# Optimization experiments

Measured on AMD Instinct MI355X. Metric: run time of the kernel, lower is better.

## Reference

```python
import jax, jax.numpy as jnp
import numpy as np

DIM = 768
HEADS = 12
HID = 3072  # mlp_ratio * dim
BATCH = 8
FRAMES = 16
GRID = 14
NTOK = GRID * GRID
LN_EPS = 1e-5
EPS = 1e-6


def setup_inputs() -> dict:
    key = jax.random.key(0)
    ks = jax.random.split(key, 8)
    w = lambda k, shape: jax.random.normal(k, shape, jnp.float32) * 0.02
    return {
        "x": jax.random.normal(ks[0], (BATCH * FRAMES, NTOK, DIM), jnp.float32),
        "ln1_w": jnp.ones((DIM,), jnp.float32),
        "ln1_b": jnp.zeros((DIM,), jnp.float32),
        "qkv_w": w(ks[1], (3 * DIM, DIM)),
        "proj_w": w(ks[2], (DIM, DIM)),
        "proj_b": jnp.zeros((DIM,), jnp.float32),
        "ln2_w": jnp.ones((DIM,), jnp.float32),
        "ln2_b": jnp.zeros((DIM,), jnp.float32),
        "fc1_w": w(ks[3], (HID, DIM)),
        "fc1_b": jnp.zeros((HID,), jnp.float32),
        "dw_w": w(ks[4], (HID, 1, 3, 3)),
        "dw_b": jnp.zeros((HID,), jnp.float32),
        "fc2_w": w(ks[5], (DIM, HID)),
        "fc2_b": jnp.zeros((DIM,), jnp.float32),
        "H": GRID,
        "W": GRID,
        "num_frames": FRAMES,
    }


def _layernorm(x, w, b):
    mu = jnp.mean(x, axis=-1, keepdims=True)
    var = jnp.mean(jnp.square(x - mu), axis=-1, keepdims=True)
    return (x - mu) * jax.lax.rsqrt(var + LN_EPS) * w + b


def _joint_ts_attention(xn, qkv_w, proj_w, proj_b, num_frames):
    # xn: (b*f, n, c)
    Bt, n, C = xn.shape
    h = HEADS
    e = C // h
    scale = e ** (-0.5)
    qkv = jnp.einsum('bnc,dc->bnd', xn, qkv_w).reshape(Bt, n, 3, h, e)
    q, k, v = qkv[:, :, 0], qkv[:, :, 1], qkv[:, :, 2]
    # ReLU feature map + scale offset
    q_ = jax.nn.relu(q) + scale
    k_ = jax.nn.relu(k) + scale
    b = Bt // num_frames
    m = num_frames * n  # joint time-space sequence length
    q_ = q_.reshape(b, m, h, e)
    k_ = k_.reshape(b, m, h, e)
    v_ = v.reshape(b, m, h, e)
    # kv_: (b, h, e, e)
    kv = jnp.einsum('bnhe,bnhd->bhed', k_, v_)
    k_sum = jnp.sum(k_, axis=1)  # (b, h, e)
    z = 1.0 / (jnp.einsum('bnhe,bhe->bnh', q_, k_sum) + EPS)  # (b, m, h)
    out = jnp.einsum('bnhe,bhed->bnhd', q_, kv) * z[..., None]  # (b, m, h, e)
    out = out.reshape(Bt, n, C)
    return jnp.einsum('bnc,dc->bnd', out, proj_w) + proj_b


def _dwconv(x, w, b, H, W):
    # x: (B, N, C) -> NCHW depthwise 3x3, pad 1
    Bn, n, c = x.shape
    xi = jnp.transpose(x, (0, 2, 1)).reshape(Bn, c, H, W)
    y = jax.lax.conv_general_dilated(
        xi, w, window_strides=(1, 1), padding=((1, 1), (1, 1)),
        dimension_numbers=('NCHW', 'OIHW', 'NCHW'), feature_group_count=c)
    y = y + b[None, :, None, None]
    return jnp.transpose(y.reshape(Bn, c, n), (0, 2, 1))


def reference(x, ln1_w, ln1_b, qkv_w, proj_w, proj_b, ln2_w, ln2_b,
              fc1_w, fc1_b, dw_w, dw_b, fc2_w, fc2_b, H, W, num_frames):
    # x = x + attn(norm1(x), num_frames)
    x = x + _joint_ts_attention(_layernorm(x, ln1_w, ln1_b), qkv_w, proj_w, proj_b, num_frames)
    # x = x + mlp(norm2(x), H, W)
    xn = _layernorm(x, ln2_w, ln2_b)
    hdn = jnp.einsum('bnc,hc->bnh', xn, fc1_w) + fc1_b
    hdn = _dwconv(hdn, dw_w, dw_b, H, W)
    hdn = jax.nn.gelu(hdn, approximate=False)
    out = jnp.einsum('bnh,ch->bnc', hdn, fc2_w) + fc2_b
    return x + out
```

## Files before the change

kernel.cpp:

```cpp
#include <hip/hip_runtime.h>

typedef unsigned short u16;
typedef unsigned int u32;

typedef __bf16 bf16x8 __attribute__((ext_vector_type(8)));
typedef float f32x4 __attribute__((ext_vector_type(4)));

#define DIM 768
#define HID 3072
#define NTOK 196
#define BT 128
#define NTOKENS (BT * NTOK)
#define MJ 3136
#define HEADS 12

#define SZ_WB   ((size_t)(2304*768 + 768*768 + 3072*768 + 768*3072) * 2)
#define SZ_XN   ((size_t)NTOKENS * DIM * 2)
#define SZ_QKV  ((size_t)NTOKENS * 2304 * 2)
#define SZ_X2   ((size_t)NTOKENS * DIM * 4)
#define SZ_HDN  ((size_t)NTOKENS * HID * 2)
#define SZ_KV   ((size_t)96 * 4096 * 4)
#define SZ_KS   ((size_t)96 * 64 * 4)
#define WS_NEED (SZ_WB + SZ_XN + SZ_QKV + SZ_X2 + SZ_HDN + SZ_KV + SZ_KS)

static void* g_buf = nullptr;

__device__ __forceinline__ float b2f(u16 u) {
  union { u32 i; float f; } x; x.i = ((u32)u) << 16; return x.f;
}
__device__ __forceinline__ u16 f2b(float f) {
  u32 x = __float_as_uint(f);
  return (u16)((x + 0x7fffu + ((x >> 16) & 1u)) >> 16);
}

__device__ __forceinline__ void gload_lds16(const u16* g, u16* l) {
  __builtin_amdgcn_global_load_lds(
      (const __attribute__((address_space(1))) u32*)g,
      (__attribute__((address_space(3))) u32*)l, 16, 0, 0);
}

__global__ __launch_bounds__(256) void cvt_f32_bf16(const float* __restrict__ in,
    u16* __restrict__ out, int n4)
{
  int i = blockIdx.x * 256 + threadIdx.x;
  if (i < n4) {
    float4 f = ((const float4*)in)[i];
    ushort4 r;
    r.x = f2b(f.x); r.y = f2b(f.y); r.z = f2b(f.z); r.w = f2b(f.w);
    ((ushort4*)out)[i] = r;
  }
}

__global__ __launch_bounds__(256) void zero_f32(float* __restrict__ p, int n) {
  int i = blockIdx.x * 256 + threadIdx.x;
  if (i < n) p[i] = 0.0f;
}

__global__ __launch_bounds__(256) void ln_kernel(const float* __restrict__ xin,
    const float* __restrict__ w, const float* __restrict__ b, u16* __restrict__ out)
{
  const int token = blockIdx.x * 4 + (threadIdx.x >> 6);
  const int lane = threadIdx.x & 63;
  float v[12];
  const float* x = xin + (size_t)token * DIM;
#pragma unroll
  for (int c = 0; c < 3; ++c) {
    float4 f = *(const float4*)(x + c * 256 + lane * 4);
    v[c*4+0] = f.x; v[c*4+1] = f.y; v[c*4+2] = f.z; v[c*4+3] = f.w;
  }
  float s = 0.f, sq = 0.f;
#pragma unroll
  for (int i = 0; i < 12; ++i) { s += v[i]; sq += v[i] * v[i]; }
#pragma unroll
  for (int off = 32; off > 0; off >>= 1) {
    s += __shfl_xor(s, off, 64);
    sq += __shfl_xor(sq, off, 64);
  }
  const float mean = s * (1.0f / 768.0f);
  const float var = sq * (1.0f / 768.0f) - mean * mean;
  const float rstd = rsqrtf(var + 1e-5f);
  u16* o = out + (size_t)token * DIM;
#pragma unroll
  for (int c = 0; c < 3; ++c) {
    float4 wv = *(const float4*)(w + c * 256 + lane * 4);
    float4 bv = *(const float4*)(b + c * 256 + lane * 4);
    ushort4 r;
    r.x = f2b((v[c*4+0] - mean) * rstd * wv.x + bv.x);
    r.y = f2b((v[c*4+1] - mean) * rstd * wv.y + bv.y);
    r.z = f2b((v[c*4+2] - mean) * rstd * wv.z + bv.z);
    r.w = f2b((v[c*4+3] - mean) * rstd * wv.w + bv.w);
    *(ushort4*)(o + c * 256 + lane * 4) = r;
  }
}

template<int MODE, int NXT, int NN, int KK>
__global__ __launch_bounds__(512, 2) void gemm8(
    const u16* __restrict__ A, const u16* __restrict__ W,
    const float* __restrict__ bias, const float* __restrict__ res,
    void* __restrict__ out)
{
  extern __shared__ char smem[];
  u16* As = (u16*)smem;
  u16* Bs = (u16*)(smem + 65536);

  const int t = threadIdx.x;
  const int l = t & 63;
  const int w = t >> 6;
  const int wm = w >> 2;
  const int wn = w & 3;

  constexpr int TOTAL = 98 * NXT;
  constexpr int Q8 = TOTAL >> 3;
  constexpr int R8 = TOTAL & 7;
  const int orig = blockIdx.x;
  const int xcd = orig & 7;
  const int idx = orig >> 3;
  const int wg = (xcd < R8) ? (xcd * (Q8 + 1) + idx)
                            : (R8 * (Q8 + 1) + (xcd - R8) * Q8 + idx);
  const int m0 = (wg / NXT) * 256;
  const int n0 = (wg % NXT) * 256;

  const int srow = w * 16 + (l >> 3);
  const int scol = ((l & 7) ^ (l >> 3)) * 8;
  const u16* gA = A + (size_t)(m0 + srow) * KK + scol;
  const u16* gB = W + (size_t)(n0 + srow) * KK + scol;
  u16* lA = As + w * 1024;
  u16* lB = Bs + w * 1024;

#define STAGE_A(bb, h, kt) do { \
    const u16* g_ = gA + (size_t)(h) * 128 * KK + (size_t)(kt) * 64; \
    u16* l_ = lA + (bb) * 16384 + (h) * 8192; \
    gload_lds16(g_, l_); \
    gload_lds16(g_ + (size_t)8 * KK, l_ + 512); } while (0)
#define STAGE_B(bb, h, kt) do { \
    const u16* g_ = gB + (size_t)(h) * 128 * KK + (size_t)(kt) * 64; \
    u16* l_ = lB + (bb) * 16384 + (h) * 8192; \
    gload_lds16(g_, l_); \
    gload_lds16(g_ + (size_t)8 * KK, l_ + 512); } while (0)

  const int lm = l & 15;
  const int qq = l >> 4;
  const int acol = (qq << 4) ^ ((l & 7) << 4);
  const int abase = (wm * 128 + lm) * 128 + acol;
  const int bbase = (wn * 64 + lm) * 128 + acol;

  f32x4 acc[8][4];
#pragma unroll
  for (int mi = 0; mi < 8; ++mi)
#pragma unroll
    for (int ni = 0; ni < 4; ++ni) acc[mi][ni] = (f32x4){0.f, 0.f, 0.f, 0.f};

  constexpr int NT = KK / 64;

  STAGE_A(0, 0, 0); STAGE_A(0, 1, 0); STAGE_B(0, 0, 0); STAGE_B(0, 1, 0);
  STAGE_A(1, 0, 1); STAGE_A(1, 1, 1);
  asm volatile("s_waitcnt vmcnt(4)" ::: "memory");
  __builtin_amdgcn_s_barrier();

  for (int ti = 0; ti < NT; ++ti) {
    const int cb = ti & 1, nb = cb ^ 1;
    const char* Ac = (const char*)As + cb * 32768;
    const char* Bc = (const char*)Bs + cb * 32768;
    bf16x8 am[4][2], b01[2][2], b23[2][2];

#pragma unroll
    for (int mi = 0; mi < 4; ++mi) {
      const int off = abase + mi * 2048;
      am[mi][0] = *(const bf16x8*)(Ac + off);
      am[mi][1] = *(const bf16x8*)(Ac + (off ^ 64));
    }
#pragma unroll
    for (int ni = 0; ni < 2; ++ni) {
      const int off = bbase + ni * 2048;
      b01[ni][0] = *(const bf16x8*)(Bc + off);
      b01[ni][1] = *(const bf16x8*)(Bc + (off ^ 64));
    }
    if (ti + 1 < NT) STAGE_B(nb, 0, ti + 1);
    asm volatile("" ::: "memory");
    __builtin_amdgcn_s_barrier();
    asm volatile("s_waitcnt lgkmcnt(0)" ::: "memory");
    __builtin_amdgcn_s_setprio(1);
#pragma unroll
    for (int mi = 0; mi < 4; ++mi)
#pragma unroll
      for (int ni = 0; ni < 2; ++ni) {
        acc[mi][ni] = __builtin_amdgcn_mfma_f32_16x16x32_bf16(am[mi][0], b01[ni][0], acc[mi][ni], 0, 0, 0);
        acc[mi][ni] = __builtin_amdgcn_mfma_f32_16x16x32_bf16(am[mi][1], b01[ni][1], acc[mi][ni], 0, 0, 0);
      }
    __builtin_amdgcn_s_setprio(0);
    asm volatile("" ::: "memory");
    __builtin_amdgcn_s_barrier();

#pragma unroll
    for (int ni = 0; ni < 2; ++ni) {
      const int off = bbase + (ni + 2) * 2048;
      b23[ni][0] = *(const bf16x8*)(Bc + off);
      b23[ni][1] = *(const bf16x8*)(Bc + (off ^ 64));
    }
    if (ti + 1 < NT) STAGE_B(nb, 1, ti + 1);
    asm volatile("" ::: "memory");
    __builtin_amdgcn_s_barrier();
    asm volatile("s_waitcnt lgkmcnt(0)" ::: "memory");
    __builtin_amdgcn_s_setprio(1);
#pragma unroll
    for (int mi = 0; mi < 4; ++mi)
#pragma unroll
      for (int ni = 0; ni < 2; ++ni) {
        acc[mi][ni + 2] = __builtin_amdgcn_mfma_f32_16x16x32_bf16(am[mi][0], b23[ni][0], acc[mi][ni + 2], 0, 0, 0);
        acc[mi][ni + 2] = __builtin_amdgcn_mfma_f32_16x16x32_bf16(am[mi][1], b23[ni][1], acc[mi][ni + 2], 0, 0, 0);
      }
    __builtin_amdgcn_s_setprio(0);
    asm volatile("" ::: "memory");
    __builtin_amdgcn_s_barrier();

#pragma unroll
    for (int mi = 0; mi < 4; ++mi) {
      const int off = abase + 8192 + mi * 2048;
      am[mi][0] = *(const bf16x8*)(Ac + off);
      am[mi][1] = *(const bf16x8*)(Ac + (off ^ 64));
    }
    asm volatile("" ::: "memory");
    __builtin_amdgcn_s_barrier();
    asm volatile("s_waitcnt lgkmcnt(0)" ::: "memory");
    __builtin_amdgcn_s_setprio(1);
#pragma unroll
    for (int mi = 0; mi < 4; ++mi)
#pragma unroll
      for (int ni = 0; ni < 2; ++ni) {
        acc[mi + 4][ni + 2] = __builtin_amdgcn_mfma_f32_16x16x32_bf16(am[mi][0], b23[ni][0], acc[mi + 4][ni + 2], 0, 0, 0);
        acc[mi + 4][ni + 2] = __builtin_amdgcn_mfma_f32_16x16x32_bf16(am[mi][1], b23[ni][1], acc[mi + 4][ni + 2], 0, 0, 0);
      }
    __builtin_amdgcn_s_setprio(0);
    asm volatile("" ::: "memory");
    __builtin_amdgcn_s_barrier();

    if (ti + 2 < NT) {
      STAGE_A(cb, 0, ti + 2);
      STAGE_A(cb, 1, ti + 2);
      asm volatile("s_waitcnt vmcnt(4)" ::: "memory");
    } else {
      asm volatile("s_waitcnt vmcnt(0)" ::: "memory");
    }
    __builtin_amdgcn_s_barrier();
    __builtin_amdgcn_s_setprio(1);
#pragma unroll
    for (int mi = 0; mi < 4; ++mi)
#pragma unroll
      for (int ni = 0; ni < 2; ++ni) {
        acc[mi + 4][ni] = __builtin_amdgcn_mfma_f32_16x16x32_bf16(am[mi][0], b01[ni][0], acc[mi + 4][ni], 0, 0, 0);
        acc[mi + 4][ni] = __builtin_amdgcn_mfma_f32_16x16x32_bf16(am[mi][1], b01[ni][1], acc[mi + 4][ni], 0, 0, 0);
      }
    __builtin_amdgcn_s_setprio(0);
    asm volatile("" ::: "memory");
    __builtin_amdgcn_s_barrier();
  }
#undef STAGE_A
#undef STAGE_B

#pragma unroll
  for (int mi = 0; mi < 8; ++mi) {
    const int rbase = m0 + wm * 128 + mi * 16 + qq * 4;
#pragma unroll
    for (int ni = 0; ni < 4; ++ni) {
      const int col = n0 + wn * 64 + ni * 16 + lm;
      float bv = 0.f;
      if (MODE != 0) bv = bias[col];
#pragma unroll
      for (int r = 0; r < 4; ++r) {
        float v = acc[mi][ni][r];
        const size_t idxo = (size_t)(rbase + r) * NN + col;
        if (MODE == 0) {
          if (col < 1536) v = fmaxf(v, 0.0f) + 0.125f;
          ((u16*)out)[idxo] = f2b(v);
        } else if (MODE == 1) {
          ((float*)out)[idxo] = v + bv + res[idxo];
        } else if (MODE == 2) {
          ((u16*)out)[idxo] = f2b(v + bv);
        } else {
          ((float*)out)[idxo] = v + bv + res[idxo];
        }
      }
    }
  }
}

__global__ __launch_bounds__(256) void kv_reduce(const u16* __restrict__ qkv,
    float* __restrict__ kv, float* __restrict__ ksum)
{
  const int bh = blockIdx.x;
  const int s = blockIdx.y;
  const int b = bh / 12, h = bh % 12;
  __shared__ __align__(16) u16 ks[64 * 64];
  __shared__ __align__(16) u16 vs[64 * 64];
  const int t = threadIdx.x;
  const int e = t & 63;
  const int dg = (t >> 6) * 16;

  float acc[16];
#pragma unroll
  for (int j = 0; j < 16; ++j) acc[j] = 0.f;
  float ksacc = 0.f;

  for (int ch = s; ch < 49; ch += 8) {
    const size_t tokbase = (size_t)b * MJ + ch * 64;
    __syncthreads();
#pragma unroll
    for (int i = 0; i < 2; ++i) {
      int c = t + i * 256;
      int row = c >> 3, eo = (c & 7) * 8;
      const u16* base = qkv + (tokbase + row) * 2304 + h * 64 + eo;
      *(uint4*)&ks[row * 64 + eo] = *(const uint4*)(base + 768);
      *(uint4*)&vs[row * 64 + eo] = *(const uint4*)(base + 1536);
    }
    __syncthreads();
    for (int m = 0; m < 64; ++m) {
      float kf = b2f(ks[m * 64 + e]);
      ksacc += kf;
      bf16x8 v0 = *(const bf16x8*)&vs[m * 64 + dg];
      bf16x8 v1 = *(const bf16x8*)&vs[m * 64 + dg + 8];
#pragma unroll
      for (int j = 0; j < 8; ++j) {
        acc[j]     += kf * (float)v0[j];
        acc[j + 8] += kf * (float)v1[j];
      }
    }
  }
  float* dst = kv + (size_t)bh * 4096 + e * 64 + dg;
#pragma unroll
  for (int j = 0; j < 16; ++j) atomicAdd(&dst[j], acc[j]);
  if (dg == 0) atomicAdd(&ksum[bh * 64 + e], ksacc);
}

__global__ __launch_bounds__(256) void attn_out(const u16* __restrict__ qkv,
    const float* __restrict__ kv, const float* __restrict__ ksum,
    u16* __restrict__ outp)
{
  const int chunk = blockIdx.x;
  const int h = blockIdx.y;
  const int b = blockIdx.z;
  __shared__ float kvs[4096];
  __shared__ float kss[64];
  __shared__ float qs[4096];
  const int t = threadIdx.x;
  const float* kvsrc = kv + (size_t)(b * 12 + h) * 4096;
  for (int i = t; i < 1024; i += 256)
    ((float4*)kvs)[i] = ((const float4*)kvsrc)[i];
  if (t < 64) kss[t] = ksum[(b * 12 + h) * 64 + t];
  __syncthreads();
  const int wv = t >> 6, lane = t & 63;
  float* qw = &qs[wv * 1024];
  const size_t tok0 = (size_t)b * MJ + chunk * 64 + wv * 16;
#pragma unroll
  for (int i = 0; i < 16; ++i) {
    float q = b2f(qkv[(tok0 + i) * 2304 + h * 64 + lane]);
    float pd = q * kss[lane];
#pragma unroll
    for (int off = 32; off > 0; off >>= 1) pd += __shfl_xor(pd, off, 64);
    qw[i * 64 + lane] = q * (1.0f / (pd + 1e-6f));
  }
  float o[16];
#pragma unroll
  for (int i = 0; i < 16; ++i) o[i] = 0.f;
  for (int e = 0; e < 64; ++e) {
    const float kvc = kvs[e * 64 + lane];
#pragma unroll
    for (int i = 0; i < 16; ++i) o[i] += qw[i * 64 + e] * kvc;
  }
#pragma unroll
  for (int i = 0; i < 16; ++i)
    outp[(tok0 + i) * 768 + h * 64 + lane] = f2b(o[i]);
}

__global__ __launch_bounds__(256) void dwconv_gelu(u16* __restrict__ hdn,
    const float* __restrict__ w, const float* __restrict__ bias)
{
  __shared__ u16 pl[196 * 136];
  const int cb = blockIdx.x;
  const int fr = blockIdx.y;
  const int t = threadIdx.x;
  const int c0 = cb * 128;
  u16* base = hdn + (size_t)fr * 196 * HID + c0;
#pragma unroll
  for (int i = 0; i < 13; ++i) {
    int idx = i * 256 + t;
    if (idx < 3136) {
      int p = idx >> 4, cq = idx & 15;
      *(uint4*)&pl[p * 136 + cq * 8] = *(const uint4*)(base + (size_t)p * HID + cq * 8);
    }
  }
  __syncthreads();
  const int pc = t & 31;
  const int pg = t >> 5;
  const int cc = pc * 4;
  float wr[36];
#pragma unroll
  for (int k = 0; k < 9; ++k)
#pragma unroll
    for (int u = 0; u < 4; ++u) wr[k * 4 + u] = w[(c0 + cc + u) * 9 + k];
  float bv[4];
#pragma unroll
  for (int u = 0; u < 4; ++u) bv[u] = bias[c0 + cc + u];

  for (int j = 0; j < 25; ++j) {
    const int p = pg + j * 8;
    if (p >= 196) break;
    const int py = p / 14, px = p % 14;
    float a0 = bv[0], a1 = bv[1], a2 = bv[2], a3 = bv[3];
#pragma unroll
    for (int ky = 0; ky < 3; ++ky) {
      int yy = py + ky - 1;
      if (yy < 0 || yy > 13) continue;
#pragma unroll
      for (int kx = 0; kx < 3; ++kx) {
        int xx = px + kx - 1;
        if (xx < 0 || xx > 13) continue;
        ushort4 tv = *(const ushort4*)&pl[(yy * 14 + xx) * 136 + cc];
        const float* wk = &wr[(ky * 3 + kx) * 4];
        a0 += wk[0] * b2f(tv.x);
        a1 += wk[1] * b2f(tv.y);
        a2 += wk[2] * b2f(tv.z);
        a3 += wk[3] * b2f(tv.w);
      }
    }
    ushort4 r;
    r.x = f2b(0.5f * a0 * (1.0f + erff(a0 * 0.70710678118654752f)));
    r.y = f2b(0.5f * a1 * (1.0f + erff(a1 * 0.70710678118654752f)));
    r.z = f2b(0.5f * a2 * (1.0f + erff(a2 * 0.70710678118654752f)));
    r.w = f2b(0.5f * a3 * (1.0f + erff(a3 * 0.70710678118654752f)));
    *(ushort4*)(base + (size_t)p * HID + cc) = r;
  }
}

static void set_gemm_attrs() {
  (void)hipFuncSetAttribute(reinterpret_cast<const void*>(&gemm8<0, 9, 2304, 768>),
                            hipFuncAttributeMaxDynamicSharedMemorySize, 131072);
  (void)hipFuncSetAttribute(reinterpret_cast<const void*>(&gemm8<1, 3, 768, 768>),
                            hipFuncAttributeMaxDynamicSharedMemorySize, 131072);
  (void)hipFuncSetAttribute(reinterpret_cast<const void*>(&gemm8<2, 12, 3072, 768>),
                            hipFuncAttributeMaxDynamicSharedMemorySize, 131072);
  (void)hipFuncSetAttribute(reinterpret_cast<const void*>(&gemm8<3, 3, 768, 3072>),
                            hipFuncAttributeMaxDynamicSharedMemorySize, 131072);
}
struct WsInit {
  WsInit() {
    (void)hipMalloc(&g_buf, WS_NEED);
    set_gemm_attrs();
  }
};
static WsInit g_wsinit;

extern "C" void kernel_launch(void* const* d_in, const int* in_sizes, int n_in,
                              void* d_out, int out_size, void* d_ws, size_t ws_size,
                              hipStream_t stream)
{
  (void)in_sizes; (void)n_in; (void)out_size;
  static bool attrs_once = [] { set_gemm_attrs(); return true; }();
  (void)attrs_once;

  const float* x     = (const float*)d_in[0];
  const float* ln1w  = (const float*)d_in[1];
  const float* ln1b  = (const float*)d_in[2];
  const float* qkvw  = (const float*)d_in[3];
  const float* projw = (const float*)d_in[4];
  const float* projb = (const float*)d_in[5];
  const float* ln2w  = (const float*)d_in[6];
  const float* ln2b  = (const float*)d_in[7];
  const float* fc1w  = (const float*)d_in[8];
  const float* fc1b  = (const float*)d_in[9];
  const float* dww   = (const float*)d_in[10];
  const float* dwb   = (const float*)d_in[11];
  const float* fc2w  = (const float*)d_in[12];
  const float* fc2b  = (const float*)d_in[13];

  char* p = (ws_size >= WS_NEED) ? (char*)d_ws : (char*)g_buf;
  u16* WQKV  = (u16*)p;   p += (size_t)2304 * 768 * 2;
  u16* WPROJ = (u16*)p;   p += (size_t)768 * 768 * 2;
  u16* WFC1  = (u16*)p;   p += (size_t)3072 * 768 * 2;
  u16* WFC2  = (u16*)p;   p += (size_t)768 * 3072 * 2;
  u16* XN    = (u16*)p;   p += SZ_XN;
  u16* QKV   = (u16*)p;   p += SZ_QKV;
  float* X2  = (float*)p; p += SZ_X2;
  u16* HDN   = (u16*)p;   p += SZ_HDN;
  float* KV  = (float*)p; p += SZ_KV;
  float* KS  = (float*)p; p += SZ_KS;

  cvt_f32_bf16<<<(2304*768/4 + 255)/256, 256, 0, stream>>>(qkvw, WQKV, 2304*768/4);
  cvt_f32_bf16<<<(768*768/4 + 255)/256, 256, 0, stream>>>(projw, WPROJ, 768*768/4);
  cvt_f32_bf16<<<(3072*768/4 + 255)/256, 256, 0, stream>>>(fc1w, WFC1, 3072*768/4);
  cvt_f32_bf16<<<(768*3072/4 + 255)/256, 256, 0, stream>>>(fc2w, WFC2, 768*3072/4);

  const int nz = 96 * 4096 + 96 * 64;
  zero_f32<<<(nz + 255) / 256, 256, 0, stream>>>(KV, nz);
  ln_kernel<<<NTOKENS / 4, 256, 0, stream>>>(x, ln1w, ln1b, XN);
  gemm8<0, 9, 2304, 768><<<98 * 9, 512, 131072, stream>>>(XN, WQKV, nullptr, nullptr, QKV);
  kv_reduce<<<dim3(96, 8), 256, 0, stream>>>(QKV, KV, KS);
  attn_out<<<dim3(49, 12, 8), 256, 0, stream>>>(QKV, KV, KS, XN);
  gemm8<1, 3, 768, 768><<<98 * 3, 512, 131072, stream>>>(XN, WPROJ, projb, x, X2);
  ln_kernel<<<NTOKENS / 4, 256, 0, stream>>>(X2, ln2w, ln2b, QKV);
  gemm8<2, 12, 3072, 768><<<98 * 12, 512, 131072, stream>>>(QKV, WFC1, fc1b, nullptr, HDN);
  dwconv_gelu<<<dim3(24, 128), 256, 0, stream>>>(HDN, dww, dwb);
  gemm8<3, 3, 768, 3072><<<98 * 3, 512, 131072, stream>>>(HDN, WFC2, fc2b, X2, (float*)d_out);
}
```

Before: 1.084 ms.

## Cut GEMM main-loop barriers from eight to two per K-tile

Restructures the double-buffered GEMM main loop so each K-tile uses two workgroup barriers instead of eight. The A fragments are split into two separate register sets (a0, a1) so all LDS reads of the current buffer can complete before one barrier, after which the next A tile is staged into that buffer. The goal is less barrier stall and better overlap of LDS reads, global staging and MFMA work. In exchange it uses more registers and depends on the reduced synchronisation still covering the LDS read/write hazards on B staging into the other buffer.

```diff
diff --git a/kernel.cpp b/kernel.cpp
--- a/kernel.cpp
+++ b/kernel.cpp
@@ -161,13 +161,13 @@
     const int cb = ti & 1, nb = cb ^ 1;
     const char* Ac = (const char*)As + cb * 32768;
     const char* Bc = (const char*)Bs + cb * 32768;
-    bf16x8 am[4][2], b01[2][2], b23[2][2];
+    bf16x8 a0[4][2], a1[4][2], b01[2][2], b23[2][2];
 
 #pragma unroll
     for (int mi = 0; mi < 4; ++mi) {
       const int off = abase + mi * 2048;
-      am[mi][0] = *(const bf16x8*)(Ac + off);
-      am[mi][1] = *(const bf16x8*)(Ac + (off ^ 64));
+      a0[mi][0] = *(const bf16x8*)(Ac + off);
+      a0[mi][1] = *(const bf16x8*)(Ac + (off ^ 64));
     }
 #pragma unroll
     for (int ni = 0; ni < 2; ++ni) {
@@ -176,20 +176,15 @@
       b01[ni][1] = *(const bf16x8*)(Bc + (off ^ 64));
     }
     if (ti + 1 < NT) STAGE_B(nb, 0, ti + 1);
-    asm volatile("" ::: "memory");
-    __builtin_amdgcn_s_barrier();
-    asm volatile("s_waitcnt lgkmcnt(0)" ::: "memory");
     __builtin_amdgcn_s_setprio(1);
 #pragma unroll
     for (int mi = 0; mi < 4; ++mi)
 #pragma unroll
       for (int ni = 0; ni < 2; ++ni) {
-        acc[mi][ni] = __builtin_amdgcn_mfma_f32_16x16x32_bf16(am[mi][0], b01[ni][0], acc[mi][ni], 0, 0, 0);
-        acc[mi][ni] = __builtin_amdgcn_mfma_f32_16x16x32_bf16(am[mi][1], b01[ni][1], acc[mi][ni], 0, 0, 0);
+        acc[mi][ni] = __builtin_amdgcn_mfma_f32_16x16x32_bf16(a0[mi][0], b01[ni][0], acc[mi][ni], 0, 0, 0);
+        acc[mi][ni] = __builtin_amdgcn_mfma_f32_16x16x32_bf16(a0[mi][1], b01[ni][1], acc[mi][ni], 0, 0, 0);
       }
     __builtin_amdgcn_s_setprio(0);
-    asm volatile("" ::: "memory");
-    __builtin_amdgcn_s_barrier();
 
 #pragma unroll
     for (int ni = 0; ni < 2; ++ni) {
@@ -198,60 +193,52 @@
       b23[ni][1] = *(const bf16x8*)(Bc + (off ^ 64));
     }
     if (ti + 1 < NT) STAGE_B(nb, 1, ti + 1);
-    asm volatile("" ::: "memory");
-    __builtin_amdgcn_s_barrier();
-    asm volatile("s_waitcnt lgkmcnt(0)" ::: "memory");
     __builtin_amdgcn_s_setprio(1);
 #pragma unroll
     for (int mi = 0; mi < 4; ++mi)
 #pragma unroll
       for (int ni = 0; ni < 2; ++ni) {
-        acc[mi][ni + 2] = __builtin_amdgcn_mfma_f32_16x16x32_bf16(am[mi][0], b23[ni][0], acc[mi][ni + 2], 0, 0, 0);
-        acc[mi][ni + 2] = __builtin_amdgcn_mfma_f32_16x16x32_bf16(am[mi][1], b23[ni][1], acc[mi][ni + 2], 0, 0, 0);
+        acc[mi][ni + 2] = __builtin_amdgcn_mfma_f32_16x16x32_bf16(a0[mi][0], b23[ni][0], acc[mi][ni + 2], 0, 0, 0);
+        acc[mi][ni + 2] = __builtin_amdgcn_mfma_f32_16x16x32_bf16(a0[mi][1], b23[ni][1], acc[mi][ni + 2], 0, 0, 0);
       }
     __builtin_amdgcn_s_setprio(0);
-    asm volatile("" ::: "memory");
-    __builtin_amdgcn_s_barrier();
 
 #pragma unroll
     for (int mi = 0; mi < 4; ++mi) {
       const int off = abase + 8192 + mi * 2048;
-      am[mi][0] = *(const bf16x8*)(Ac + off);
-      am[mi][1] = *(const bf16x8*)(Ac + (off ^ 64));
-    }
-    asm volatile("" ::: "memory");
+      a1[mi][0] = *(const bf16x8*)(Ac + off);
+      a1[mi][1] = *(const bf16x8*)(Ac + (off ^ 64));
+    }
+    __builtin_amdgcn_s_setprio(1);
+#pragma unroll
+    for (int mi = 0; mi < 4; ++mi)
+#pragma unroll
+      for (int ni = 0; ni < 2; ++ni) {
+        acc[mi + 4][ni + 2] = __builtin_amdgcn_mfma_f32_16x16x32_bf16(a1[mi][0], b23[ni][0], acc[mi + 4][ni + 2], 0, 0, 0);
+        acc[mi + 4][ni + 2] = __builtin_amdgcn_mfma_f32_16x16x32_bf16(a1[mi][1], b23[ni][1], acc[mi + 4][ni + 2], 0, 0, 0);
+      }
+    __builtin_amdgcn_s_setprio(0);
+
+    asm volatile("s_waitcnt lgkmcnt(0)" ::: "memory");
     __builtin_amdgcn_s_barrier();
-    asm volatile("s_waitcnt lgkmcnt(0)" ::: "memory");
+
+    if (ti + 2 < NT) { STAGE_A(cb, 0, ti + 2); STAGE_A(cb, 1, ti + 2); }
+
     __builtin_amdgcn_s_setprio(1);
 #pragma unroll
     for (int mi = 0; mi < 4; ++mi)
 #pragma unroll
       for (int ni = 0; ni < 2; ++ni) {
-        acc[mi + 4][ni + 2] = __builtin_amdgcn_mfma_f32_16x16x32_bf16(am[mi][0], b23[ni][0], acc[mi + 4][ni + 2], 0, 0, 0);
-        acc[mi + 4][ni + 2] = __builtin_amdgcn_mfma_f32_16x16x32_bf16(am[mi][1], b23[ni][1], acc[mi + 4][ni + 2], 0, 0, 0);
+        acc[mi + 4][ni] = __builtin_amdgcn_mfma_f32_16x16x32_bf16(a1[mi][0], b01[ni][0], acc[mi + 4][ni], 0, 0, 0);
+        acc[mi + 4][ni] = __builtin_amdgcn_mfma_f32_16x16x32_bf16(a1[mi][1], b01[ni][1], acc[mi + 4][ni], 0, 0, 0);
       }
     __builtin_amdgcn_s_setprio(0);
-    asm volatile("" ::: "memory");
-    __builtin_amdgcn_s_barrier();
 
     if (ti + 2 < NT) {
-      STAGE_A(cb, 0, ti + 2);
-      STAGE_A(cb, 1, ti + 2);
       asm volatile("s_waitcnt vmcnt(4)" ::: "memory");
     } else {
       asm volatile("s_waitcnt vmcnt(0)" ::: "memory");
     }
-    __builtin_amdgcn_s_barrier();
-    __builtin_amdgcn_s_setprio(1);
-#pragma unroll
-    for (int mi = 0; mi < 4; ++mi)
-#pragma unroll
-      for (int ni = 0; ni < 2; ++ni) {
-        acc[mi + 4][ni] = __builtin_amdgcn_mfma_f32_16x16x32_bf16(am[mi][0], b01[ni][0], acc[mi + 4][ni], 0, 0, 0);
-        acc[mi + 4][ni] = __builtin_amdgcn_mfma_f32_16x16x32_bf16(am[mi][1], b01[ni][1], acc[mi + 4][ni], 0, 0, 0);
-      }
-    __builtin_amdgcn_s_setprio(0);
-    asm volatile("" ::: "memory");
     __builtin_amdgcn_s_barrier();
   }
 #undef STAGE_A
```

New measurement: 1.067 ms. No clear change (-1.6%).
